# Kernel tuning notes

Measured on AMD Instinct MI355X. Metric: run time of the kernel, lower is better.

## Reference

```python
import jax, jax.numpy as jnp
import numpy as np

P = 1024
D_FF = 4096
TGT = 4096
SRC = 4096


def _ln(x, g, b, eps=1e-5):
    mu = jnp.mean(x, axis=-1, keepdims=True)
    var = jnp.mean((x - mu) ** 2, axis=-1, keepdims=True)
    return (x - mu) / jnp.sqrt(var + eps) * g + b


def setup_inputs() -> dict:
    key = jax.random.key(0)
    ks = jax.random.split(key, 32)
    s = 1.0 / np.sqrt(P)
    sf = 1.0 / np.sqrt(D_FF)
    d = {
        "Y": jax.random.normal(ks[0], (TGT, P), jnp.float32),
        "Xp": jax.random.normal(ks[1], (SRC, P), jnp.float32),
        # self-attn projections (Linear: y = x @ W + b, W stored [in, out])
        "wq1": jax.random.uniform(ks[2], (P, P), jnp.float32, -s, s),
        "bq1": jnp.zeros((P,), jnp.float32),
        "wk1": jax.random.uniform(ks[3], (P, P), jnp.float32, -s, s),
        "bk1": jnp.zeros((P,), jnp.float32),
        "wv1": jax.random.uniform(ks[4], (P, P), jnp.float32, -s, s),
        "bv1": jnp.zeros((P,), jnp.float32),
        "w0": jax.random.uniform(ks[5], (P, P), jnp.float32, -s, s),
        "b0": jnp.zeros((P,), jnp.float32),
        "g1": jnp.ones((P,), jnp.float32),
        "be1": jnp.zeros((P,), jnp.float32),
        # cross-attn projections
        "wq2": jax.random.uniform(ks[6], (P, P), jnp.float32, -s, s),
        "bq2": jnp.zeros((P,), jnp.float32),
        "wk2": jax.random.uniform(ks[7], (P, P), jnp.float32, -s, s),
        "bk2": jnp.zeros((P,), jnp.float32),
        "wv2": jax.random.uniform(ks[8], (P, P), jnp.float32, -s, s),
        "bv2": jnp.zeros((P,), jnp.float32),
        "w1": jax.random.uniform(ks[9], (P, P), jnp.float32, -s, s),
        "b1": jnp.zeros((P,), jnp.float32),
        "g2": jnp.ones((P,), jnp.float32),
        "be2": jnp.zeros((P,), jnp.float32),
        # FFN
        "w2": jax.random.uniform(ks[10], (P, D_FF), jnp.float32, -s, s),
        "b2": jnp.zeros((D_FF,), jnp.float32),
        "w3": jax.random.uniform(ks[11], (D_FF, P), jnp.float32, -sf, sf),
        "b3": jnp.zeros((P,), jnp.float32),
        "g3": jnp.ones((P,), jnp.float32),
        "be3": jnp.zeros((P,), jnp.float32),
    }
    return d


def reference(Y, Xp, wq1, bq1, wk1, bk1, wv1, bv1, w0, b0, g1, be1,
              wq2, bq2, wk2, bk2, wv2, bv2, w1, b1, g2, be2,
              w2, b2, w3, b3, g3, be3):
    m = Y.shape[0]
    scale = 1.0 / jnp.sqrt(jnp.asarray(P, Y.dtype))
    # --- masked self-attention on Y ---
    Q = Y @ wq1 + bq1            # [m, p]
    K = Y @ wk1 + bk1
    V = Y @ wv1 + bv1
    S = (Q @ K.T) * scale        # [m, m]
    causal = jnp.tril(jnp.ones((m, m), bool))
    S = jnp.where(causal, S, jnp.asarray(-1e9, S.dtype))
    A = jax.nn.softmax(S, axis=-1)
    T1 = (A @ V) @ w0 + b0
    U1 = _ln(Y + T1, g1, be1)
    # --- cross-attention with encoder output Xp ---
    Q = U1 @ wq2 + bq2           # [m, p]
    K = Xp @ wk2 + bk2           # [n, p]
    V = Xp @ wv2 + bv2
    S = (Q @ K.T) * scale        # [m, n]
    A = jax.nn.softmax(S, axis=-1)
    T2 = (A @ V) @ w1 + b1
    U2 = _ln(U1 + T2, g2, be2)
    # --- position-wise FFN ---
    Z = jax.nn.relu(U2 @ w2 + b2) @ w3 + b3
    U3 = _ln(U2 + Z, g3, be3)
    return U3
```

## Files before the change

kernel.cpp:

```cpp
#include <hip/hip_runtime.h>
#include <hip/hip_bf16.h>

typedef __bf16 bf16x8 __attribute__((ext_vector_type(8)));
typedef __bf16 bf16x4 __attribute__((ext_vector_type(4)));
typedef float f32x4 __attribute__((ext_vector_type(4)));

#define AS1P(p) ((__attribute__((address_space(1))) void*)(void*)(p))
#define AS3P(p) ((__attribute__((address_space(3))) void*)(p))

__global__ __launch_bounds__(256) void gemm_bt(
    const __hip_bfloat16* __restrict__ A, int lda,
    const __hip_bfloat16* __restrict__ Bt, int ldb,
    int M, int N, int K, int ldc,
    const float* __restrict__ bias, int bias_mode,
    float scale,
    const float* __restrict__ residual,
    int relu, int causal_skip, int trapezoid, int ksplit,
    float* __restrict__ Cf, __hip_bfloat16* __restrict__ Cb,
    int nsplit1, const __hip_bfloat16* __restrict__ A2,
    const __hip_bfloat16* __restrict__ Bt2, int ldb2, int ldc2,
    const float* __restrict__ bias2, __hip_bfloat16* __restrict__ Cb2)
{
    int nb = blockIdx.x;
    if (nsplit1 && nb >= nsplit1) {
        A = A2; Bt = Bt2; ldb = ldb2; ldc = ldc2; bias = bias2;
        Cb = Cb2; Cf = nullptr; residual = nullptr;
        nb -= nsplit1;
    }
    const int m_base = blockIdx.y * 128;
    const int n_base = nb * 128;
    if (causal_skip && (n_base > m_base + 127)) return;
    int Kend = K;
    if (trapezoid) { int kl = m_base + 128; Kend = kl < K ? kl : K; }
    int kb = 0, ke = Kend;
    if (ksplit) {
        kb = blockIdx.z * ksplit;
        int k2 = kb + ksplit; ke = k2 < Kend ? k2 : Kend;
        if (kb >= ke) return;
        Cb += (size_t)blockIdx.z * M * ldc;
        Cf = nullptr;
    }
    const int nt = (ke - kb) >> 6;

    __shared__ __align__(16) __hip_bfloat16 Al[2][128 * 64];
    __shared__ __align__(16) __hip_bfloat16 Bl[2][128 * 64];

    const int tid  = threadIdx.x;
    const int lane = tid & 63;
    const int wave = tid >> 6;
    const int wm = (wave >> 1) * 64;
    const int wn = (wave & 1) * 64;

    f32x4 acc[4][4];
#pragma unroll
    for (int i = 0; i < 4; ++i)
#pragma unroll
        for (int j = 0; j < 4; ++j) acc[i][j] = f32x4{0.f, 0.f, 0.f, 0.f};

    const bool isA = wave < 2;
    const __hip_bfloat16* G = isA ? (A + (size_t)m_base * lda) : (Bt + (size_t)n_base * ldb);
    const int ldg = isA ? lda : ldb;
    const int qbase = (wave & 1) * 8;
    const int rsub  = lane >> 3;
    const int cx    = (lane & 7) ^ rsub;
    const size_t grow = (size_t)(qbase * 8 + rsub) * ldg + (size_t)cx * 8 + kb;

    const int lrow = lane & 15;
    const int csel = lane >> 4;
    const int l7   = lane & 7;

#define ISSUE_TILE(KT, STG)                                                      \
    {                                                                            \
        const __hip_bfloat16* g = G + grow + (size_t)(KT) * 64;                  \
        __hip_bfloat16* dst = (isA ? &Al[STG][0] : &Bl[STG][0]) + qbase * 512;   \
        _Pragma("unroll")                                                        \
        for (int q = 0; q < 8; ++q) {                                            \
            __builtin_amdgcn_global_load_lds(AS1P(g), AS3P(dst), 16, 0, 0);      \
            g += (size_t)8 * ldg; dst += 512;                                    \
        }                                                                        \
    }

    ISSUE_TILE(0, 0)

    for (int kt = 0; kt < nt; ++kt) {
        const int cur = kt & 1;
        if (kt + 1 < nt) {
            ISSUE_TILE(kt + 1, cur ^ 1)
            __builtin_amdgcn_s_waitcnt(0x0F78);
        } else {
            __builtin_amdgcn_s_waitcnt(0x0F70);
        }
        __builtin_amdgcn_sched_barrier(0);
        __builtin_amdgcn_s_barrier();

#pragma unroll
        for (int ks = 0; ks < 2; ++ks) {
            const int cphys = ((ks * 4 + csel) ^ l7) * 8;
            bf16x8 af[4], bfv[4];
#pragma unroll
            for (int i = 0; i < 4; ++i)
                af[i] = *(const bf16x8*)&Al[cur][(wm + i * 16 + lrow) * 64 + cphys];
#pragma unroll
            for (int j = 0; j < 4; ++j)
                bfv[j] = *(const bf16x8*)&Bl[cur][(wn + j * 16 + lrow) * 64 + cphys];
#pragma unroll
            for (int i = 0; i < 4; ++i)
#pragma unroll
                for (int j = 0; j < 4; ++j)
                    acc[i][j] = __builtin_amdgcn_mfma_f32_16x16x32_bf16(af[i], bfv[j], acc[i][j], 0, 0, 0);
        }
        __builtin_amdgcn_s_waitcnt(0xC07F);
        __builtin_amdgcn_sched_barrier(0);
        __builtin_amdgcn_s_barrier();
    }
#undef ISSUE_TILE

    const int r0 = (lane >> 4) * 4;
    const int c0 = lane & 15;
#pragma unroll
    for (int i = 0; i < 4; ++i) {
#pragma unroll
        for (int j = 0; j < 4; ++j) {
            const int col = n_base + wn + j * 16 + c0;
#pragma unroll
            for (int r = 0; r < 4; ++r) {
                const int row = m_base + wm + i * 16 + r0 + r;
                float v = acc[i][j][r] * scale;
                if (bias_mode == 1) v += bias[col];
                else if (bias_mode == 2) v += bias[row];
                if (relu) v = fmaxf(v, 0.f);
                const size_t idx = (size_t)row * ldc + col;
                if (residual) v += residual[idx];
                if (Cf) Cf[idx] = v;
                else    Cb[idx] = __float2bfloat16(v);
            }
        }
    }
}

__global__ __launch_bounds__(256) void reduce_k_kernel(
    const __hip_bfloat16* __restrict__ Pb, int M, int N, int nsplit, int KC, int trapK,
    const float* __restrict__ bias, const float* __restrict__ residual,
    float* __restrict__ Cf, __hip_bfloat16* __restrict__ Cb)
{
    const int idx = blockIdx.x * 256 + threadIdx.x;
    const int nv = N >> 2;
    const int row = idx / nv;
    if (row >= M) return;
    const int c4 = (idx - row * nv) * 4;
    int nc = nsplit;
    if (trapK) {
        int kend = (row & ~127) + 128; if (kend > trapK) kend = trapK;
        nc = (kend + KC - 1) / KC;
    }
    float s0 = 0.f, s1 = 0.f, s2 = 0.f, s3 = 0.f;
    for (int c = 0; c < nc; ++c) {
        const bf16x4 p = *(const bf16x4*)(Pb + ((size_t)c * M + row) * N + c4);
        s0 += (float)p[0]; s1 += (float)p[1]; s2 += (float)p[2]; s3 += (float)p[3];
    }
    if (bias) {
        const f32x4 b = *(const f32x4*)(bias + c4);
        s0 += b[0]; s1 += b[1]; s2 += b[2]; s3 += b[3];
    }
    if (residual) {
        const f32x4 rv = *(const f32x4*)(residual + (size_t)row * N + c4);
        s0 += rv[0]; s1 += rv[1]; s2 += rv[2]; s3 += rv[3];
    }
    if (Cf) { f32x4 o = {s0, s1, s2, s3}; *(f32x4*)(Cf + (size_t)row * N + c4) = o; }
    else {
        bf16x4 o = { (__bf16)s0, (__bf16)s1, (__bf16)s2, (__bf16)s3 };
        *(bf16x4*)(Cb + (size_t)row * N + c4) = o;
    }
}

__global__ __launch_bounds__(256) void convert_bf16_kernel(
    const float* __restrict__ x, __hip_bfloat16* __restrict__ y, int n4)
{
    const int i = blockIdx.x * 256 + threadIdx.x;
    if (i >= n4) return;
    const float4 v = ((const float4*)x)[i];
    bf16x4 o = { (__bf16)v.x, (__bf16)v.y, (__bf16)v.z, (__bf16)v.w };
    *(bf16x4*)(y + (size_t)i * 4) = o;
}

__global__ __launch_bounds__(256) void transpose_convert_kernel(
    const float* __restrict__ W, __hip_bfloat16* __restrict__ Wt, int K, int N)
{
    __shared__ float t[32][33];
    const int k0 = blockIdx.y * 32;
    const int n0 = blockIdx.x * 32;
    const int tx = threadIdx.x;
    for (int i = threadIdx.y; i < 32; i += 8)
        t[i][tx] = W[(size_t)(k0 + i) * N + n0 + tx];
    __syncthreads();
    for (int i = threadIdx.y; i < 32; i += 8)
        Wt[(size_t)(n0 + i) * K + k0 + tx] = __float2bfloat16(t[tx][i]);
}

__global__ __launch_bounds__(256) void transpose_bf16_kernel(
    const __hip_bfloat16* __restrict__ src, int ls,
    __hip_bfloat16* __restrict__ dst, int ld)
{
    __shared__ __hip_bfloat16 t[32][33];
    const int r0 = blockIdx.y * 32;
    const int c0 = blockIdx.x * 32;
    const int tx = threadIdx.x;
    for (int i = threadIdx.y; i < 32; i += 8)
        t[i][tx] = src[(size_t)(r0 + i) * ls + c0 + tx];
    __syncthreads();
    for (int i = threadIdx.y; i < 32; i += 8)
        dst[(size_t)(c0 + i) * ld + r0 + tx] = t[tx][i];
}

__global__ __launch_bounds__(256) void softmax_kernel(
    const __hip_bfloat16* __restrict__ S, __hip_bfloat16* __restrict__ A, int N, int causal)
{
    __shared__ float sm[4];
    const int row = blockIdx.x;
    const int tid = threadIdx.x;
    const int limit = causal ? (row + 1) : N;
    const int zlimit = causal ? (((row & ~127) + 128) < N ? ((row & ~127) + 128) : N) : N;
    const __hip_bfloat16* Srow = S + (size_t)row * N;
    __hip_bfloat16* Arow = A + (size_t)row * N;
    const int nv = limit >> 2;

    float m = -3.0e38f;
    for (int v = tid; v < nv; v += 256) {
        const bf16x4 x = *(const bf16x4*)(Srow + (size_t)v * 4);
        m = fmaxf(m, fmaxf(fmaxf((float)x[0], (float)x[1]), fmaxf((float)x[2], (float)x[3])));
    }
    for (int j = (nv << 2) + tid; j < limit; j += 256) m = fmaxf(m, (float)Srow[j]);
#pragma unroll
    for (int o = 32; o; o >>= 1) m = fmaxf(m, __shfl_down(m, o));
    if ((tid & 63) == 0) sm[tid >> 6] = m;
    __syncthreads();
    m = fmaxf(fmaxf(sm[0], sm[1]), fmaxf(sm[2], sm[3]));
    __syncthreads();

    float s = 0.f;
    for (int v = tid; v < nv; v += 256) {
        const bf16x4 x = *(const bf16x4*)(Srow + (size_t)v * 4);
        s += __expf((float)x[0] - m) + __expf((float)x[1] - m)
           + __expf((float)x[2] - m) + __expf((float)x[3] - m);
    }
    for (int j = (nv << 2) + tid; j < limit; j += 256) s += __expf((float)Srow[j] - m);
#pragma unroll
    for (int o = 32; o; o >>= 1) s += __shfl_down(s, o);
    if ((tid & 63) == 0) sm[tid >> 6] = s;
    __syncthreads();
    s = sm[0] + sm[1] + sm[2] + sm[3];
    const float inv = 1.f / s;

    for (int v = tid; v < nv; v += 256) {
        const bf16x4 x = *(const bf16x4*)(Srow + (size_t)v * 4);
        bf16x4 o = { (__bf16)(__expf((float)x[0] - m) * inv), (__bf16)(__expf((float)x[1] - m) * inv),
                     (__bf16)(__expf((float)x[2] - m) * inv), (__bf16)(__expf((float)x[3] - m) * inv) };
        *(bf16x4*)(Arow + (size_t)v * 4) = o;
    }
    for (int j = (nv << 2) + tid; j < limit; j += 256)
        Arow[j] = __float2bfloat16(__expf((float)Srow[j] - m) * inv);
    const __hip_bfloat16 z = __float2bfloat16(0.f);
    for (int j = limit + tid; j < zlimit; j += 256) Arow[j] = z;
}

__global__ __launch_bounds__(256) void layernorm_kernel(
    const float* __restrict__ X, const float* __restrict__ g, const float* __restrict__ b,
    float* __restrict__ outF, __hip_bfloat16* __restrict__ outB)
{
    __shared__ float sm[8];
    const int row = blockIdx.x;
    const int tid = threadIdx.x;
    const float4 v = ((const float4*)(X + (size_t)row * 1024))[tid];
    float s  = v.x + v.y + v.z + v.w;
    float ss = v.x * v.x + v.y * v.y + v.z * v.z + v.w * v.w;
#pragma unroll
    for (int o = 32; o; o >>= 1) { s += __shfl_down(s, o); ss += __shfl_down(ss, o); }
    if ((tid & 63) == 0) { sm[tid >> 6] = s; sm[4 + (tid >> 6)] = ss; }
    __syncthreads();
    s  = sm[0] + sm[1] + sm[2] + sm[3];
    ss = sm[4] + sm[5] + sm[6] + sm[7];
    const float mu   = s * (1.f / 1024.f);
    const float var  = ss * (1.f / 1024.f) - mu * mu;
    const float rstd = rsqrtf(var + 1e-5f);
    const float4 gv = ((const float4*)g)[tid];
    const float4 bv = ((const float4*)b)[tid];
    float4 o;
    o.x = (v.x - mu) * rstd * gv.x + bv.x;
    o.y = (v.y - mu) * rstd * gv.y + bv.y;
    o.z = (v.z - mu) * rstd * gv.z + bv.z;
    o.w = (v.w - mu) * rstd * gv.w + bv.w;
    ((float4*)(outF + (size_t)row * 1024))[tid] = o;
    if (outB) {
        bf16x4 ob = { (__bf16)o.x, (__bf16)o.y, (__bf16)o.z, (__bf16)o.w };
        *(bf16x4*)(outB + (size_t)row * 1024 + (size_t)tid * 4) = ob;
    }
}

extern "C" void kernel_launch(void* const* d_in, const int* in_sizes, int n_in,
                              void* d_out, int out_size, void* d_ws, size_t ws_size,
                              hipStream_t stream)
{
    const int M = 4096, Pd = 1024, DFF = 4096, NS = 4096;
    const size_t MB = 1024 * 1024;

    const float* Y   = (const float*)d_in[0];
    const float* Xp  = (const float*)d_in[1];
    const float* wq1 = (const float*)d_in[2];  const float* bq1 = (const float*)d_in[3];
    const float* wk1 = (const float*)d_in[4];  const float* bk1 = (const float*)d_in[5];
    const float* wv1 = (const float*)d_in[6];  const float* bv1 = (const float*)d_in[7];
    const float* w0  = (const float*)d_in[8];  const float* b0  = (const float*)d_in[9];
    const float* g1  = (const float*)d_in[10]; const float* be1 = (const float*)d_in[11];
    const float* wq2 = (const float*)d_in[12]; const float* bq2 = (const float*)d_in[13];
    const float* wk2 = (const float*)d_in[14]; const float* bk2 = (const float*)d_in[15];
    const float* wv2 = (const float*)d_in[16]; const float* bv2 = (const float*)d_in[17];
    const float* w1  = (const float*)d_in[18]; const float* b1  = (const float*)d_in[19];
    const float* g2  = (const float*)d_in[20]; const float* be2 = (const float*)d_in[21];
    const float* w2  = (const float*)d_in[22]; const float* b2  = (const float*)d_in[23];
    const float* w3  = (const float*)d_in[24]; const float* b3  = (const float*)d_in[25];
    const float* g3  = (const float*)d_in[26]; const float* be3 = (const float*)d_in[27];

    char* ws = (char*)d_ws;
    __hip_bfloat16* Ybf   = (__hip_bfloat16*)(ws + 0 * MB);
    __hip_bfloat16* Ubf   = (__hip_bfloat16*)(ws + 0 * MB);
    __hip_bfloat16* Xpbf  = (__hip_bfloat16*)(ws + 8 * MB);
    __hip_bfloat16* AVbf  = (__hip_bfloat16*)(ws + 8 * MB);
    __hip_bfloat16* Qbf   = (__hip_bfloat16*)(ws + 8 * MB);
    __hip_bfloat16* wqkv1t= (__hip_bfloat16*)(ws + 16 * MB);
    __hip_bfloat16* w0t   = (__hip_bfloat16*)(ws + 22 * MB);
    __hip_bfloat16* wq2t  = (__hip_bfloat16*)(ws + 24 * MB);
    __hip_bfloat16* wkv2t = (__hip_bfloat16*)(ws + 26 * MB);
    __hip_bfloat16* w1t   = (__hip_bfloat16*)(ws + 30 * MB);
    __hip_bfloat16* w2t   = (__hip_bfloat16*)(ws + 32 * MB);
    __hip_bfloat16* w3t   = (__hip_bfloat16*)(ws + 40 * MB);
    float*          bqkv1 = (float*)(ws + 48 * MB);
    float*          bkv2  = (float*)(ws + 48 * MB + 512 * 1024);
    __hip_bfloat16* QKV1  = (__hip_bfloat16*)(ws + 49 * MB);
    __hip_bfloat16* KV2   = (__hip_bfloat16*)(ws + 73 * MB);
    __hip_bfloat16* Vt    = (__hip_bfloat16*)(ws + 89 * MB);
    __hip_bfloat16* Sb    = (__hip_bfloat16*)(ws + 97 * MB);
    __hip_bfloat16* Pb    = (__hip_bfloat16*)(ws + 97 * MB);
    __hip_bfloat16* Abf   = (__hip_bfloat16*)(ws + 161 * MB);
    float*          Xres  = (float*)(ws + 193 * MB);
    float*          Uf    = (float*)(ws + 209 * MB);
    float*          Out   = (float*)d_out;
    if (ws_size < 225 * MB) return;

    auto cvt = [&](const float* src, __hip_bfloat16* dst, int n) {
        convert_bf16_kernel<<<dim3(n / 1024), dim3(256), 0, stream>>>(src, dst, n / 4);
    };
    auto tconv = [&](const float* W, __hip_bfloat16* Wt, int K, int N) {
        transpose_convert_kernel<<<dim3(N / 32, K / 32), dim3(32, 8), 0, stream>>>(W, Wt, K, N);
    };
    auto tbf = [&](const __hip_bfloat16* src, int ls, __hip_bfloat16* dst, int ld, int R, int C) {
        transpose_bf16_kernel<<<dim3(C / 32, R / 32), dim3(32, 8), 0, stream>>>(src, ls, dst, ld);
    };
    auto gemm = [&](const __hip_bfloat16* A, int lda, const __hip_bfloat16* Bt, int ldb,
                    int Mm, int Nn, int Kk, int ldc,
                    const float* bias, int bmode, float scale, const float* res,
                    int relu, int causal, int trap, int ksplit,
                    float* Cf, __hip_bfloat16* Cb) {
        const int nz = ksplit ? (Kk + ksplit - 1) / ksplit : 1;
        gemm_bt<<<dim3(Nn / 128, Mm / 128, nz), dim3(256), 0, stream>>>(
            A, lda, Bt, ldb, Mm, Nn, Kk, ldc, bias, bmode, scale, res, relu, causal, trap, ksplit,
            Cf, Cb, 0, nullptr, nullptr, 0, 0, nullptr, nullptr);
    };
    auto reduce = [&](const __hip_bfloat16* P, int Mm, int Nn, int nsplit, int KC, int trapK,
                      const float* bias, const float* res, float* Cf, __hip_bfloat16* Cb) {
        reduce_k_kernel<<<dim3(Mm * Nn / 1024), dim3(256), 0, stream>>>(
            P, Mm, Nn, nsplit, KC, trapK, bias, res, Cf, Cb);
    };

    const float scl = 0.03125f;

    cvt(Y,  Ybf,  M * Pd);
    cvt(Xp, Xpbf, NS * Pd);
    tconv(wq1, wqkv1t,            Pd, Pd);
    tconv(wk1, wqkv1t + Pd * Pd,  Pd, Pd);
    tconv(wv1, wqkv1t + 2*Pd*Pd,  Pd, Pd);
    tconv(w0,  w0t,  Pd, Pd);
    tconv(wq2, wq2t, Pd, Pd);
    tconv(wk2, wkv2t,           Pd, Pd);
    tconv(wv2, wkv2t + Pd * Pd, Pd, Pd);
    tconv(w1,  w1t,  Pd, Pd);
    tconv(w2, w2t, Pd, DFF);
    tconv(w3, w3t, DFF, Pd);
    hipMemcpyAsync(bqkv1,            bq1, Pd * 4, hipMemcpyDeviceToDevice, stream);
    hipMemcpyAsync(bqkv1 + Pd,       bk1, Pd * 4, hipMemcpyDeviceToDevice, stream);
    hipMemcpyAsync(bqkv1 + 2 * Pd,   bv1, Pd * 4, hipMemcpyDeviceToDevice, stream);
    hipMemcpyAsync(bkv2,             bk2, Pd * 4, hipMemcpyDeviceToDevice, stream);
    hipMemcpyAsync(bkv2 + Pd,        bv2, Pd * 4, hipMemcpyDeviceToDevice, stream);

    gemm_bt<<<dim3(40, 32, 1), dim3(256), 0, stream>>>(
        Ybf, Pd, wqkv1t, Pd, M, 3072, Pd, 3072, bqkv1, 1, 1.f, nullptr, 0, 0, 0, 0,
        nullptr, QKV1,
        24, Xpbf, wkv2t, Pd, 2048, bkv2, KV2);

    tbf(QKV1 + 2048, 3072, Vt, M, M, Pd);
    gemm(QKV1, 3072, QKV1 + 1024, 3072, M, M, Pd, M,
         nullptr, 0, scl, nullptr, 0, 1, 0, 0, nullptr, Sb);
    softmax_kernel<<<dim3(M), dim3(256), 0, stream>>>(Sb, Abf, M, 1);
    gemm(Abf, M, Vt, M, M, Pd, M, Pd,
         nullptr, 0, 1.f, nullptr, 0, 0, 1, 1024, nullptr, Pb);
    reduce(Pb, M, Pd, 4, 1024, M, nullptr, nullptr, nullptr, AVbf);
    gemm(AVbf, Pd, w0t, Pd, M, Pd, Pd, Pd, b0, 1, 1.f, Y, 0, 0, 0, 0, Xres, nullptr);
    layernorm_kernel<<<dim3(M), dim3(256), 0, stream>>>(Xres, g1, be1, Uf, Ubf);

    gemm(Ubf, Pd, wq2t, Pd, M, Pd, Pd, Pd, bq2, 1, 1.f, nullptr, 0, 0, 0, 0, nullptr, Qbf);
    tbf(KV2 + 1024, 2048, Vt, NS, NS, Pd);
    gemm(Qbf, Pd, KV2, 2048, M, NS, Pd, NS,
         nullptr, 0, scl, nullptr, 0, 0, 0, 0, nullptr, Sb);
    softmax_kernel<<<dim3(M), dim3(256), 0, stream>>>(Sb, Abf, NS, 0);
    gemm(Abf, NS, Vt, NS, M, Pd, NS, Pd,
         nullptr, 0, 1.f, nullptr, 0, 0, 0, 1024, nullptr, Pb);
    reduce(Pb, M, Pd, 4, 1024, 0, nullptr, nullptr, nullptr, AVbf);
    gemm(AVbf, Pd, w1t, Pd, M, Pd, Pd, Pd, b1, 1, 1.f, Uf, 0, 0, 0, 0, Xres, nullptr);
    layernorm_kernel<<<dim3(M), dim3(256), 0, stream>>>(Xres, g2, be2, Uf, Ubf);

    gemm(Ubf, Pd, w2t, Pd, M, DFF, Pd, DFF, b2, 1, 1.f, nullptr, 1, 0, 0, 0, nullptr, Abf);
    gemm(Abf, DFF, w3t, DFF, M, Pd, DFF, Pd,
         nullptr, 0, 1.f, nullptr, 0, 0, 0, 1024, nullptr, Pb);
    reduce(Pb, M, Pd, 4, 1024, 0, b3, Uf, Xres, nullptr);
    layernorm_kernel<<<dim3(M), dim3(256), 0, stream>>>(Xres, g3, be3, Out, nullptr);
}
```

Before: 802.6 us.

## Switch GEMM to triple-buffered LDS with BK=32 tiles and occupancy hint

The bf16 GEMM kernel now uses a K-tile of 32 instead of 64 and a three-stage LDS ring, so two tiles are in flight while one is being computed. The XOR swizzle and waitcnt values are adjusted for the new layout, and launch_bounds gains a minimum of 3 blocks per CU. The goal is to hide global-to-LDS latency better and raise occupancy through lower LDS use per block. The cost is twice as many barriers per unit of K and fewer MFMAs between syncs, plus possible register pressure from the occupancy hint.

```diff
diff --git a/kernel.cpp b/kernel.cpp
--- a/kernel.cpp
+++ b/kernel.cpp
@@ -8,7 +8,7 @@
 #define AS1P(p) ((__attribute__((address_space(1))) void*)(void*)(p))
 #define AS3P(p) ((__attribute__((address_space(3))) void*)(p))
 
-__global__ __launch_bounds__(256) void gemm_bt(
+__global__ __launch_bounds__(256, 3) void gemm_bt(
     const __hip_bfloat16* __restrict__ A, int lda,
     const __hip_bfloat16* __restrict__ Bt, int ldb,
     int M, int N, int K, int ldc,
@@ -40,10 +40,9 @@
         Cb += (size_t)blockIdx.z * M * ldc;
         Cf = nullptr;
     }
-    const int nt = (ke - kb) >> 6;
-
-    __shared__ __align__(16) __hip_bfloat16 Al[2][128 * 64];
-    __shared__ __align__(16) __hip_bfloat16 Bl[2][128 * 64];
+    const int nt = (ke - kb) >> 5;
+
+    __shared__ __align__(16) __hip_bfloat16 Lds[3][8192];
 
     const int tid  = threadIdx.x;
     const int lane = tid & 63;
@@ -60,58 +59,60 @@
     const bool isA = wave < 2;
     const __hip_bfloat16* G = isA ? (A + (size_t)m_base * lda) : (Bt + (size_t)n_base * ldb);
     const int ldg = isA ? lda : ldb;
-    const int qbase = (wave & 1) * 8;
-    const int rsub  = lane >> 3;
-    const int cx    = (lane & 7) ^ rsub;
-    const size_t grow = (size_t)(qbase * 8 + rsub) * ldg + (size_t)cx * 8 + kb;
+    const int q0 = (wave & 1) * 4;
+    const int rsub = lane >> 2;
+    const int cx   = (lane & 3) ^ ((lane >> 3) & 3);
+    const size_t grow = (size_t)(q0 * 16 + rsub) * ldg + (size_t)cx * 8 + kb;
+    const int ldsoff = (isA ? 0 : 4096) + q0 * 512;
 
     const int lrow = lane & 15;
-    const int csel = lane >> 4;
-    const int l7   = lane & 7;
+    const int cph  = ((lane >> 4) ^ ((lrow >> 1) & 3)) * 8;
 
 #define ISSUE_TILE(KT, STG)                                                      \
     {                                                                            \
-        const __hip_bfloat16* g = G + grow + (size_t)(KT) * 64;                  \
-        __hip_bfloat16* dst = (isA ? &Al[STG][0] : &Bl[STG][0]) + qbase * 512;   \
+        const __hip_bfloat16* g = G + grow + (size_t)(KT) * 32;                  \
+        __hip_bfloat16* dst = &Lds[STG][ldsoff];                                 \
         _Pragma("unroll")                                                        \
-        for (int q = 0; q < 8; ++q) {                                            \
+        for (int q = 0; q < 4; ++q) {                                            \
             __builtin_amdgcn_global_load_lds(AS1P(g), AS3P(dst), 16, 0, 0);      \
-            g += (size_t)8 * ldg; dst += 512;                                    \
+            g += (size_t)16 * ldg; dst += 512;                                   \
         }                                                                        \
     }
 
     ISSUE_TILE(0, 0)
-
+    if (nt > 1) ISSUE_TILE(1, 1)
+
+    int s2 = 2;
     for (int kt = 0; kt < nt; ++kt) {
-        const int cur = kt & 1;
-        if (kt + 1 < nt) {
-            ISSUE_TILE(kt + 1, cur ^ 1)
+        const int cur = (kt == 0) ? 0 : (s2 + 1 >= 3 ? s2 - 2 : s2 + 1);
+        if (kt + 2 < nt) {
+            ISSUE_TILE(kt + 2, s2)
             __builtin_amdgcn_s_waitcnt(0x0F78);
+        } else if (kt + 1 < nt) {
+            __builtin_amdgcn_s_waitcnt(0x0F74);
         } else {
             __builtin_amdgcn_s_waitcnt(0x0F70);
         }
         __builtin_amdgcn_sched_barrier(0);
         __builtin_amdgcn_s_barrier();
 
-#pragma unroll
-        for (int ks = 0; ks < 2; ++ks) {
-            const int cphys = ((ks * 4 + csel) ^ l7) * 8;
-            bf16x8 af[4], bfv[4];
-#pragma unroll
-            for (int i = 0; i < 4; ++i)
-                af[i] = *(const bf16x8*)&Al[cur][(wm + i * 16 + lrow) * 64 + cphys];
+        bf16x8 af[4], bfv[4];
+#pragma unroll
+        for (int i = 0; i < 4; ++i)
+            af[i] = *(const bf16x8*)&Lds[cur][(wm + i * 16 + lrow) * 32 + cph];
+#pragma unroll
+        for (int j = 0; j < 4; ++j)
+            bfv[j] = *(const bf16x8*)&Lds[cur][4096 + (wn + j * 16 + lrow) * 32 + cph];
+#pragma unroll
+        for (int i = 0; i < 4; ++i)
 #pragma unroll
             for (int j = 0; j < 4; ++j)
-                bfv[j] = *(const bf16x8*)&Bl[cur][(wn + j * 16 + lrow) * 64 + cphys];
-#pragma unroll
-            for (int i = 0; i < 4; ++i)
-#pragma unroll
-                for (int j = 0; j < 4; ++j)
-                    acc[i][j] = __builtin_amdgcn_mfma_f32_16x16x32_bf16(af[i], bfv[j], acc[i][j], 0, 0, 0);
-        }
+                acc[i][j] = __builtin_amdgcn_mfma_f32_16x16x32_bf16(af[i], bfv[j], acc[i][j], 0, 0, 0);
+
         __builtin_amdgcn_s_waitcnt(0xC07F);
         __builtin_amdgcn_sched_barrier(0);
         __builtin_amdgcn_s_barrier();
+        s2 = (s2 + 1 >= 3) ? 0 : s2 + 1;
     }
 #undef ISSUE_TILE
 
```

After: 812.6 us. Within noise of the previous version (+1.2%).
